# Optimization experiments

Measured on AMD Instinct MI355X. Metric: run time of the kernel, lower is better.

The kernel has to match this reference:

```python
import jax, jax.numpy as jnp
import numpy as np

N_ATOMS = 8000
N_PAIRS = 80000
NF_IN = 32
NF_OUT = 32
N_DIST = 16
N_COMP = 4      # l_max=1: [l=0 (1), l=1 (3)] tensor components
N_INV = 2       # _invariant_counts[(2, 1)]
MIND_SOFT = 0.85
MAXD_SOFT = 5.0
HARD_CUTOFF = 6.5
GN_EPS = 1e-5


def _sensitivity(dist, mu, sigma):
    # HIP-NN style inverse-distance Gaussians with smooth cos^2 cutoff.
    inv_d = 1.0 / dist                                   # (P,)
    base = jnp.exp(-0.5 * ((inv_d[:, None] - mu) / sigma) ** 2)  # (P, n_dist)
    cut = jnp.where(dist < HARD_CUTOFF,
                    jnp.cos(0.5 * jnp.pi * dist / HARD_CUTOFF) ** 2, 0.0)
    return base * cut[:, None]


def setup_inputs() -> dict:
    key = jax.random.key(0)
    ks = jax.random.split(key, 10)
    in_features = jax.random.normal(ks[0], (N_ATOMS, NF_IN), jnp.float32)
    pair_first = jnp.sort(jax.random.randint(ks[1], (N_PAIRS,), 0, N_ATOMS))
    pair_second = jax.random.randint(ks[2], (N_PAIRS,), 0, N_ATOMS)
    dist_pairs = (0.5 + (HARD_CUTOFF - 0.5)
                  * jax.random.uniform(ks[3], (N_PAIRS,), jnp.float32))
    tensor_rhats = jax.random.normal(ks[4], (N_PAIRS, N_COMP), jnp.float32)
    # learned params
    sens_mu = jnp.linspace(1.0 / MAXD_SOFT, 1.0 / MIND_SOFT, N_DIST).astype(jnp.float32)
    sens_sigma = jnp.full((N_DIST,), float(sens_mu[1] - sens_mu[0]), jnp.float32)
    s_int = (2.0 / (N_DIST * NF_IN + NF_OUT)) ** 0.5
    int_weights = s_int * jax.random.normal(ks[5], (N_DIST, NF_OUT, NF_IN), jnp.float32)
    s_self = (2.0 / (NF_IN + NF_OUT)) ** 0.5
    selfint_w = s_self * jax.random.normal(ks[6], (NF_OUT, NF_IN), jnp.float32)
    selfint_b = jnp.zeros((NF_OUT,), jnp.float32)
    s_mix = (2.0 / (N_INV * NF_OUT + NF_OUT)) ** 0.5
    mixing_weights = s_mix * jax.random.normal(ks[7], (NF_OUT, N_INV, NF_OUT), jnp.float32)
    gn_weight = jnp.ones((N_INV * NF_OUT,), jnp.float32)
    gn_bias = jnp.zeros((N_INV * NF_OUT,), jnp.float32)
    return {
        "in_features": in_features, "tensor_rhats": tensor_rhats,
        "dist_pairs": dist_pairs, "int_weights": int_weights,
        "selfint_w": selfint_w, "selfint_b": selfint_b,
        "mixing_weights": mixing_weights, "gn_weight": gn_weight,
        "gn_bias": gn_bias, "sens_mu": sens_mu, "sens_sigma": sens_sigma,
        "pair_first": pair_first, "pair_second": pair_second,
    }


def reference(in_features, tensor_rhats, dist_pairs, int_weights,
              selfint_w, selfint_b, mixing_weights, gn_weight, gn_bias,
              sens_mu, sens_sigma, pair_first, pair_second):
    n_atoms = in_features.shape[0]
    # self interaction (Linear)
    self_part = in_features @ selfint_w.T + selfint_b          # (N, nf_out)
    # tensor sensitivities: (P, n_comp, n_dist) -> flat (P, n_comp*n_dist)
    sense = _sensitivity(dist_pairs, sens_mu, sens_sigma)      # (P, n_dist)
    sense_flat = (tensor_rhats[:, :, None] * sense[:, None, :]).reshape(
        -1, N_COMP * N_DIST)
    # envsum: env[a, s, f] = sum_{p: pair_first[p]=a} sense_flat[p, s] * feat[pair_second[p], f]
    feat_j = in_features[pair_second]                          # (P, nf_in)
    contrib = sense_flat[:, :, None] * feat_j[:, None, :]      # (P, S, nf_in)
    env = jax.ops.segment_sum(contrib, pair_first, num_segments=n_atoms)
    # interaction weights contraction
    w_rs = jnp.transpose(int_weights, (0, 2, 1)).reshape(N_DIST * NF_IN, NF_OUT)
    env_rs = env.reshape(n_atoms * N_COMP, N_DIST * NF_IN)
    tf = (env_rs @ w_rs).reshape(n_atoms, N_COMP, NF_OUT)
    tf = jnp.transpose(tf, (0, 2, 1))                          # (N, nf_out, n_comp)
    # HopInvariantLayer (n_max=2, l_max=1): [l=0 scalar, |l=1 vector|^2]
    invariants = jnp.stack(
        [tf[..., 0], jnp.sum(tf[..., 1:] ** 2, axis=-1)], axis=-1)  # (N, nf_out, 2)
    # GroupNorm over channels (n_inv groups of nf_out channels)
    x = jnp.transpose(invariants, (0, 2, 1))                   # (N, n_inv, nf_out)
    mean = jnp.mean(x, axis=-1, keepdims=True)
    var = jnp.var(x, axis=-1, keepdims=True)
    xn = (x - mean) / jnp.sqrt(var + GN_EPS)
    xn = xn * gn_weight.reshape(N_INV, NF_OUT) + gn_bias.reshape(N_INV, NF_OUT)
    norm_inv = jnp.transpose(xn, (0, 2, 1)).reshape(n_atoms, NF_OUT * N_INV)
    mix = norm_inv @ mixing_weights.reshape(NF_OUT * N_INV, NF_OUT)
    return mix + self_part
```

## Files before the change

kernel.cpp:

```cpp
#include <hip/hip_runtime.h>
#include <hip/hip_bf16.h>
#include <stdint.h>

#define GN_EPS 1e-5f

typedef __fp16 half2_t __attribute__((ext_vector_type(2)));
typedef __fp16 v8h __attribute__((ext_vector_type(8)));
typedef float v4f __attribute__((ext_vector_type(4)));
union U32H2 { uint32_t u; half2_t h; };
union U4V8 { uint4 u; v8h h; };
union UF { uint32_t u; float f; };

__device__ __forceinline__ float ldin(const void* p, int i, bool bf) {
    if (bf) {
        UF c; c.u = ((uint32_t)((const uint16_t*)p)[i]) << 16;
        return c.f;
    }
    return ((const float*)p)[i];
}

__device__ __forceinline__ uint16_t f2bf(float x) {
    union { float f; uint32_t u; } c; c.f = x;
    uint32_t u = c.u;
    return (uint16_t)((u + 0x7FFFu + ((u >> 16) & 1u)) >> 16);
}

__device__ __forceinline__ bool detect_bf16(const void* gnw) {
    uint32_t det = *(const uint32_t*)gnw;
    return (det >> 16) == (det & 0xFFFFu);
}

__device__ __forceinline__ uint32_t pkh2(float lo, float hi) {
    U32H2 u; u.h = __builtin_amdgcn_cvt_pkrtz(lo, hi); return u.u;
}

__global__ __launch_bounds__(256) void k0_prep(
    const void* __restrict__ intw, const void* __restrict__ selfw,
    const void* __restrict__ selfb, const void* __restrict__ mw,
    const void* __restrict__ gnw, const void* __restrict__ gnb,
    const void* __restrict__ mu, const void* __restrict__ sig,
    const int* __restrict__ pf,
    int* __restrict__ seg, uint32_t* __restrict__ Wmf,
    uint32_t* __restrict__ selfh, float* __restrict__ mwT,
    float* __restrict__ gnwf, float* __restrict__ gnbf,
    float* __restrict__ selfbf, float* __restrict__ muf,
    float* __restrict__ isgf, int n_atoms, int n_pairs)
{
    const bool bf = detect_bf16(gnw);
    const int tid = blockIdx.x * 256 + threadIdx.x;

    if (tid < n_pairs) {
        int a0 = pf[tid];
        if (tid == 0) { for (int a = 0; a <= a0; ++a) seg[a] = 0; }
        if (tid + 1 < n_pairs) {
            int a1 = pf[tid + 1];
            for (int a = a0 + 1; a <= a1; ++a) seg[a] = tid + 1;
        } else {
            for (int a = a0 + 1; a <= n_atoms; ++a) seg[a] = n_pairs;
        }
    }
    if (tid < 8192) {
        int fp = tid & 15, d = (tid >> 4) & 15, o = tid >> 8;
        float wlo = ldin(intw, (d * 32 + o) * 32 + 2 * fp, bf);
        float whi = ldin(intw, (d * 32 + o) * 32 + 2 * fp + 1, bf);
        Wmf[tid] = pkh2(wlo, whi);
    }
    if (tid < 512) {
        int fp = tid & 15, o = tid >> 4;
        selfh[tid] = pkh2(ldin(selfw, o * 32 + 2 * fp, bf),
                          ldin(selfw, o * 32 + 2 * fp + 1, bf));
    }
    if (tid < 2048) {
        int k = tid & 63, o = tid >> 6;
        mwT[tid] = ldin(mw, k * 32 + o, bf);
    }
    if (tid < 64) { gnwf[tid] = ldin(gnw, tid, bf); gnbf[tid] = ldin(gnb, tid, bf); }
    if (tid < 32) selfbf[tid] = ldin(selfb, tid, bf);
    if (tid < 16) { muf[tid] = ldin(mu, tid, bf); isgf[tid] = 1.0f / ldin(sig, tid, bf); }
}

template <bool BF>
__device__ __forceinline__ void ldfeat8(const void* feat, int j, int fq, float fj[8]) {
    if (BF) {
        uint4 q = *(const uint4*)((const uint16_t*)feat + (size_t)j * 32 + fq * 8);
        uint32_t qd[4] = {q.x, q.y, q.z, q.w};
#pragma unroll
        for (int k = 0; k < 4; ++k) {
            UF lo, hi; lo.u = qd[k] << 16; hi.u = qd[k] & 0xFFFF0000u;
            fj[2 * k] = lo.f; fj[2 * k + 1] = hi.f;
        }
    } else {
        const float4* fr = (const float4*)((const float*)feat + (size_t)j * 32) + fq * 2;
        float4 a = fr[0], b = fr[1];
        fj[0] = a.x; fj[1] = a.y; fj[2] = a.z; fj[3] = a.w;
        fj[4] = b.x; fj[5] = b.y; fj[6] = b.z; fj[7] = b.w;
    }
}

template <bool BF>
__device__ __forceinline__ void pair_phase(
    const void* __restrict__ feat, const void* __restrict__ rhats,
    const void* __restrict__ dists, const int* __restrict__ ps,
    int s, int e, int fq, float mu_d, float isg_d, float (&env)[4][8])
{
    for (int p = s; p < e; p += 4) {
        int jj[4]; float4 rc[4]; float invd[4];
#pragma unroll
        for (int i = 0; i < 4; ++i) {
            int pi = (p + i < e) ? p + i : e - 1;
            jj[i] = ps[pi];
            float dist, r0, r1, r2, r3;
            if (BF) {
                UF d16; d16.u = ((uint32_t)((const uint16_t*)dists)[pi]) << 16;
                dist = d16.f;
                uint2 rv = *(const uint2*)((const uint16_t*)rhats + 4 * pi);
                UF e0, e1, e2, e3;
                e0.u = rv.x << 16; e1.u = rv.x & 0xFFFF0000u;
                e2.u = rv.y << 16; e3.u = rv.y & 0xFFFF0000u;
                r0 = e0.f; r1 = e1.f; r2 = e2.f; r3 = e3.f;
            } else {
                dist = ((const float*)dists)[pi];
                float4 rv = ((const float4*)rhats)[pi];
                r0 = rv.x; r1 = rv.y; r2 = rv.z; r3 = rv.w;
            }
            float cd = __cosf(0.2416609733530613f * dist);
            float cut = (dist < 6.5f) ? cd * cd : 0.0f;
            if (p + i >= e) cut = 0.0f;
            rc[i] = make_float4(r0 * cut, r1 * cut, r2 * cut, r3 * cut);
            invd[i] = __builtin_amdgcn_rcpf(dist);
        }
        float fj[4][8];
#pragma unroll
        for (int i = 0; i < 4; ++i) ldfeat8<BF>(feat, jj[i], fq, fj[i]);
#pragma unroll
        for (int i = 0; i < 4; ++i) {
            float x = (invd[i] - mu_d) * isg_d;
            float sd = __expf(-0.5f * x * x);
            float t0 = sd * rc[i].x, t1 = sd * rc[i].y;
            float t2 = sd * rc[i].z, t3 = sd * rc[i].w;
#pragma unroll
            for (int fl = 0; fl < 8; ++fl) {
                env[0][fl] = fmaf(t0, fj[i][fl], env[0][fl]);
                env[1][fl] = fmaf(t1, fj[i][fl], env[1][fl]);
                env[2][fl] = fmaf(t2, fj[i][fl], env[2][fl]);
                env[3][fl] = fmaf(t3, fj[i][fl], env[3][fl]);
            }
        }
    }
}

__global__ __launch_bounds__(256, 5) void k2_main(
    const int* __restrict__ seg, const uint32_t* __restrict__ Wmf,
    const uint32_t* __restrict__ selfh, const float* __restrict__ mwT,
    const void* __restrict__ feat, const void* __restrict__ rhats,
    const void* __restrict__ dists, const int* __restrict__ ps,
    const float* __restrict__ gnwf, const float* __restrict__ gnbf,
    const float* __restrict__ selfbf, const float* __restrict__ muf,
    const float* __restrict__ isgf, const void* __restrict__ gnw,
    void* __restrict__ out, int n_atoms)
{
    __shared__ uint32_t envs[16 * 256];
    __shared__ float tfs[4 * 32 * 4];
    __shared__ float selfs[4][32];
    __shared__ float xns[4][64];

    const bool bf = detect_bf16(gnw);
    const int t = threadIdx.x, wv = t >> 6, lane = t & 63;
    const int a0 = blockIdx.x * 4;
    int a = a0 + wv;
    const bool astore = (a < n_atoms);
    if (!astore) a = n_atoms - 1;

    const int dD = lane >> 2, fq = lane & 3;
    const float mu_d = muf[dD], isg_d = isgf[dD];

    float env[4][8];
#pragma unroll
    for (int c = 0; c < 4; ++c)
#pragma unroll
        for (int fl = 0; fl < 8; ++fl) env[c][fl] = 0.0f;

    const int s = seg[a], e = seg[a + 1];
    if (bf) pair_phase<true >(feat, rhats, dists, ps, s, e, fq, mu_d, isg_d, env);
    else    pair_phase<false>(feat, rhats, dists, ps, s, e, fq, mu_d, isg_d, env);

    {
        const int ci = dD * 4 + fq;
#pragma unroll
        for (int c = 0; c < 4; ++c) {
            int m = wv * 4 + c;
            uint4 w;
            w.x = pkh2(env[c][0], env[c][1]);
            w.y = pkh2(env[c][2], env[c][3]);
            w.z = pkh2(env[c][4], env[c][5]);
            w.w = pkh2(env[c][6], env[c][7]);
            *(uint4*)&envs[m * 256 + ((ci ^ m) << 2)] = w;
        }
    }
    __syncthreads();

    const int mrow = lane & 15, quad = lane >> 4;
    const int tile = wv >> 1;
    if ((wv & 1) == 0) {
        v4f acc = {0.f, 0.f, 0.f, 0.f};
        const uint4* wb = (const uint4*)Wmf + ((tile * 16 + mrow) * 64 + quad);
#pragma unroll
        for (int kk = 0; kk < 16; ++kk) {
            int cia = kk * 4 + quad;
            U4V8 Af, Bf;
            Af.u = *(const uint4*)&envs[mrow * 256 + ((cia ^ mrow) << 2)];
            Bf.u = wb[kk * 4];
            acc = __builtin_amdgcn_mfma_f32_16x16x32_f16(Af.h, Bf.h, acc, 0, 0, 0);
        }
        float4 st; st.x = acc[0]; st.y = acc[1]; st.z = acc[2]; st.w = acc[3];
        *(float4*)&tfs[(quad * 32 + tile * 16 + mrow) * 4] = st;
    } else {
        int ar = a0 + (mrow < 4 ? mrow : 0);
        if (ar >= n_atoms) ar = n_atoms - 1;
        U4V8 Af, Bf;
        if (bf) {
            uint4 q = *(const uint4*)((const uint16_t*)feat + (size_t)ar * 32 + quad * 8);
            uint32_t qd[4] = {q.x, q.y, q.z, q.w};
            uint32_t r[4];
#pragma unroll
            for (int k = 0; k < 4; ++k) {
                UF lo, hi; lo.u = qd[k] << 16; hi.u = qd[k] & 0xFFFF0000u;
                r[k] = pkh2(lo.f, hi.f);
            }
            Af.u = make_uint4(r[0], r[1], r[2], r[3]);
        } else {
            const float4* fp4 = (const float4*)((const float*)feat + (size_t)ar * 32 + quad * 8);
            float4 x = fp4[0], y = fp4[1];
            Af.u = make_uint4(pkh2(x.x, x.y), pkh2(x.z, x.w),
                              pkh2(y.x, y.y), pkh2(y.z, y.w));
        }
        Bf.u = *(const uint4*)(selfh + (tile * 16 + mrow) * 16 + quad * 4);
        v4f acc = {0.f, 0.f, 0.f, 0.f};
        acc = __builtin_amdgcn_mfma_f32_16x16x32_f16(Af.h, Bf.h, acc, 0, 0, 0);
        if (quad == 0) {
#pragma unroll
            for (int r = 0; r < 4; ++r)
                selfs[r][tile * 16 + mrow] = acc[r];
        }
    }
    __syncthreads();

    const int o = lane & 31, half = lane >> 5;
    float4 tf = *(const float4*)&tfs[(wv * 32 + o) * 4];
    float inv0 = tf.x;
    float inv1 = tf.y * tf.y + tf.z * tf.z + tf.w * tf.w;

    float s0 = inv0, q0 = inv0 * inv0, s1 = inv1, q1 = inv1 * inv1;
#pragma unroll
    for (int m = 16; m >= 1; m >>= 1) {
        s0 += __shfl_xor(s0, m, 32);
        q0 += __shfl_xor(q0, m, 32);
        s1 += __shfl_xor(s1, m, 32);
        q1 += __shfl_xor(q1, m, 32);
    }
    float mean0 = s0 * (1.f / 32.f), mean1 = s1 * (1.f / 32.f);
    float var0 = q0 * (1.f / 32.f) - mean0 * mean0;
    float var1 = q1 * (1.f / 32.f) - mean1 * mean1;
    float xn0 = (inv0 - mean0) * rsqrtf(var0 + GN_EPS);
    float xn1 = (inv1 - mean1) * rsqrtf(var1 + GN_EPS);
    xn0 = xn0 * gnwf[o] + gnbf[o];
    xn1 = xn1 * gnwf[32 + o] + gnbf[32 + o];

    if (half == 0) *(float2*)&xns[wv][2 * o] = make_float2(xn0, xn1);

    float mix = 0.0f;
    const float4* mrow4 = (const float4*)(mwT + o * 64);
#pragma unroll
    for (int c = 0; c < 16; ++c) {
        float4 xk = *(const float4*)&xns[wv][c * 4];
        float4 w4 = mrow4[c];
        mix = fmaf(xk.x, w4.x, mix);
        mix = fmaf(xk.y, w4.y, mix);
        mix = fmaf(xk.z, w4.z, mix);
        mix = fmaf(xk.w, w4.w, mix);
    }

    float res = mix + selfs[wv][o] + selfbf[o];
    if (half == 0 && astore) {
        if (bf) ((uint16_t*)out)[a * 32 + o] = f2bf(res);
        else    ((float*)out)[a * 32 + o]    = res;
    }
}

extern "C" void kernel_launch(void* const* d_in, const int* in_sizes, int n_in,
                              void* d_out, int out_size, void* d_ws, size_t ws_size,
                              hipStream_t stream) {
    const void* feat  = d_in[0];
    const void* rhats = d_in[1];
    const void* dists = d_in[2];
    const void* intw  = d_in[3];
    const void* selfw = d_in[4];
    const void* selfb = d_in[5];
    const void* mw    = d_in[6];
    const void* gnw   = d_in[7];
    const void* gnb   = d_in[8];
    const void* mu    = d_in[9];
    const void* sig   = d_in[10];
    const int* pf     = (const int*)d_in[11];
    const int* ps     = (const int*)d_in[12];

    const int n_pairs = in_sizes[11];
    const int n_atoms = in_sizes[0] / 32;

    char* ws = (char*)d_ws;
    int*      seg    = (int*)(ws + 0);
    uint32_t* Wmf    = (uint32_t*)(ws + 32768);
    uint32_t* selfh  = (uint32_t*)(ws + 65536);
    float*    mwT    = (float*)(ws + 69632);
    float*    gnwf   = (float*)(ws + 77824);
    float*    gnbf   = (float*)(ws + 78080);
    float*    selfbf = (float*)(ws + 78336);
    float*    muf    = (float*)(ws + 78464);
    float*    isgf   = (float*)(ws + 78528);

    int thr = n_pairs < 8192 ? 8192 : n_pairs;
    hipLaunchKernelGGL(k0_prep, dim3((thr + 255) / 256), dim3(256), 0, stream,
                       intw, selfw, selfb, mw, gnw, gnb, mu, sig, pf,
                       seg, Wmf, selfh, mwT, gnwf, gnbf, selfbf, muf, isgf,
                       n_atoms, n_pairs);
    hipLaunchKernelGGL(k2_main, dim3((n_atoms + 3) / 4), dim3(256), 0, stream,
                       seg, Wmf, selfh, mwT, feat, rhats, dists, ps,
                       gnwf, gnbf, selfbf, muf, isgf, gnw, d_out, n_atoms);
}
```

Before: 116.8 us.

## Fuse prep kernel into main kernel with binary-search segment bounds

Removes the separate prep kernel. Each wave now finds its atom's pair range by binary search over the sorted pair_first array, and weights are read and converted to fp16 directly from the raw inputs inside the main kernel. This drops one launch and the serial dependency between the two kernels. In exchange it adds redundant per-block weight conversion, global loads in the MFMA loop, a less efficient scalar mixing loop, and lowers the occupancy hint from 5 to 4.

```diff
diff --git a/kernel.cpp b/kernel.cpp
--- a/kernel.cpp
+++ b/kernel.cpp
@@ -34,49 +34,24 @@
     U32H2 u; u.h = __builtin_amdgcn_cvt_pkrtz(lo, hi); return u.u;
 }
 
-__global__ __launch_bounds__(256) void k0_prep(
-    const void* __restrict__ intw, const void* __restrict__ selfw,
-    const void* __restrict__ selfb, const void* __restrict__ mw,
-    const void* __restrict__ gnw, const void* __restrict__ gnb,
-    const void* __restrict__ mu, const void* __restrict__ sig,
-    const int* __restrict__ pf,
-    int* __restrict__ seg, uint32_t* __restrict__ Wmf,
-    uint32_t* __restrict__ selfh, float* __restrict__ mwT,
-    float* __restrict__ gnwf, float* __restrict__ gnbf,
-    float* __restrict__ selfbf, float* __restrict__ muf,
-    float* __restrict__ isgf, int n_atoms, int n_pairs)
-{
-    const bool bf = detect_bf16(gnw);
-    const int tid = blockIdx.x * 256 + threadIdx.x;
-
-    if (tid < n_pairs) {
-        int a0 = pf[tid];
-        if (tid == 0) { for (int a = 0; a <= a0; ++a) seg[a] = 0; }
-        if (tid + 1 < n_pairs) {
-            int a1 = pf[tid + 1];
-            for (int a = a0 + 1; a <= a1; ++a) seg[a] = tid + 1;
-        } else {
-            for (int a = a0 + 1; a <= n_atoms; ++a) seg[a] = n_pairs;
-        }
-    }
-    if (tid < 8192) {
-        int fp = tid & 15, d = (tid >> 4) & 15, o = tid >> 8;
-        float wlo = ldin(intw, (d * 32 + o) * 32 + 2 * fp, bf);
-        float whi = ldin(intw, (d * 32 + o) * 32 + 2 * fp + 1, bf);
-        Wmf[tid] = pkh2(wlo, whi);
-    }
-    if (tid < 512) {
-        int fp = tid & 15, o = tid >> 4;
-        selfh[tid] = pkh2(ldin(selfw, o * 32 + 2 * fp, bf),
-                          ldin(selfw, o * 32 + 2 * fp + 1, bf));
-    }
-    if (tid < 2048) {
-        int k = tid & 63, o = tid >> 6;
-        mwT[tid] = ldin(mw, k * 32 + o, bf);
-    }
-    if (tid < 64) { gnwf[tid] = ldin(gnw, tid, bf); gnbf[tid] = ldin(gnb, tid, bf); }
-    if (tid < 32) selfbf[tid] = ldin(selfb, tid, bf);
-    if (tid < 16) { muf[tid] = ldin(mu, tid, bf); isgf[tid] = 1.0f / ldin(sig, tid, bf); }
+template <bool BF>
+__device__ __forceinline__ uint4 ldrow16(const void* w, int row, int quad) {
+    if (BF) {
+        uint4 q = *(const uint4*)((const uint16_t*)w + (size_t)row * 32 + quad * 8);
+        uint32_t qd[4] = {q.x, q.y, q.z, q.w};
+        uint32_t r[4];
+#pragma unroll
+        for (int k = 0; k < 4; ++k) {
+            UF lo, hi; lo.u = qd[k] << 16; hi.u = qd[k] & 0xFFFF0000u;
+            r[k] = pkh2(lo.f, hi.f);
+        }
+        return make_uint4(r[0], r[1], r[2], r[3]);
+    } else {
+        const float4* f = (const float4*)((const float*)w + (size_t)row * 32 + quad * 8);
+        float4 x = f[0], y = f[1];
+        return make_uint4(pkh2(x.x, x.y), pkh2(x.z, x.w),
+                          pkh2(y.x, y.y), pkh2(y.z, y.w));
+    }
 }
 
 template <bool BF>
@@ -149,15 +124,15 @@
     }
 }
 
-__global__ __launch_bounds__(256, 5) void k2_main(
-    const int* __restrict__ seg, const uint32_t* __restrict__ Wmf,
-    const uint32_t* __restrict__ selfh, const float* __restrict__ mwT,
+__global__ __launch_bounds__(256, 4) void k_all(
     const void* __restrict__ feat, const void* __restrict__ rhats,
-    const void* __restrict__ dists, const int* __restrict__ ps,
-    const float* __restrict__ gnwf, const float* __restrict__ gnbf,
-    const float* __restrict__ selfbf, const float* __restrict__ muf,
-    const float* __restrict__ isgf, const void* __restrict__ gnw,
-    void* __restrict__ out, int n_atoms)
+    const void* __restrict__ dists, const void* __restrict__ intw,
+    const void* __restrict__ selfw, const void* __restrict__ selfb,
+    const void* __restrict__ mw, const void* __restrict__ gnw,
+    const void* __restrict__ gnb, const void* __restrict__ mu,
+    const void* __restrict__ sig, const int* __restrict__ pf,
+    const int* __restrict__ ps, void* __restrict__ out,
+    int n_atoms, int n_pairs)
 {
     __shared__ uint32_t envs[16 * 256];
     __shared__ float tfs[4 * 32 * 4];
@@ -171,8 +146,21 @@
     const bool astore = (a < n_atoms);
     if (!astore) a = n_atoms - 1;
 
+    int s, e;
+    {
+        int target = a + (lane & 1);
+        int lo = 0, hi = n_pairs;
+        while (lo < hi) {
+            int mid = (lo + hi) >> 1;
+            if (pf[mid] < target) lo = mid + 1; else hi = mid;
+        }
+        s = __shfl(lo, 0, 64);
+        e = __shfl(lo, 1, 64);
+    }
+
     const int dD = lane >> 2, fq = lane & 3;
-    const float mu_d = muf[dD], isg_d = isgf[dD];
+    const float mu_d = ldin(mu, dD, bf);
+    const float isg_d = 1.0f / ldin(sig, dD, bf);
 
     float env[4][8];
 #pragma unroll
@@ -180,7 +168,6 @@
 #pragma unroll
         for (int fl = 0; fl < 8; ++fl) env[c][fl] = 0.0f;
 
-    const int s = seg[a], e = seg[a + 1];
     if (bf) pair_phase<true >(feat, rhats, dists, ps, s, e, fq, mu_d, isg_d, env);
     else    pair_phase<false>(feat, rhats, dists, ps, s, e, fq, mu_d, isg_d, env);
 
@@ -201,46 +188,32 @@
 
     const int mrow = lane & 15, quad = lane >> 4;
     const int tile = wv >> 1;
+    const int og = tile * 16 + mrow;
     if ((wv & 1) == 0) {
         v4f acc = {0.f, 0.f, 0.f, 0.f};
-        const uint4* wb = (const uint4*)Wmf + ((tile * 16 + mrow) * 64 + quad);
 #pragma unroll
         for (int kk = 0; kk < 16; ++kk) {
             int cia = kk * 4 + quad;
             U4V8 Af, Bf;
             Af.u = *(const uint4*)&envs[mrow * 256 + ((cia ^ mrow) << 2)];
-            Bf.u = wb[kk * 4];
+            Bf.u = bf ? ldrow16<true >(intw, kk * 32 + og, quad)
+                      : ldrow16<false>(intw, kk * 32 + og, quad);
             acc = __builtin_amdgcn_mfma_f32_16x16x32_f16(Af.h, Bf.h, acc, 0, 0, 0);
         }
         float4 st; st.x = acc[0]; st.y = acc[1]; st.z = acc[2]; st.w = acc[3];
-        *(float4*)&tfs[(quad * 32 + tile * 16 + mrow) * 4] = st;
+        *(float4*)&tfs[(quad * 32 + og) * 4] = st;
     } else {
         int ar = a0 + (mrow < 4 ? mrow : 0);
         if (ar >= n_atoms) ar = n_atoms - 1;
         U4V8 Af, Bf;
-        if (bf) {
-            uint4 q = *(const uint4*)((const uint16_t*)feat + (size_t)ar * 32 + quad * 8);
-            uint32_t qd[4] = {q.x, q.y, q.z, q.w};
-            uint32_t r[4];
-#pragma unroll
-            for (int k = 0; k < 4; ++k) {
-                UF lo, hi; lo.u = qd[k] << 16; hi.u = qd[k] & 0xFFFF0000u;
-                r[k] = pkh2(lo.f, hi.f);
-            }
-            Af.u = make_uint4(r[0], r[1], r[2], r[3]);
-        } else {
-            const float4* fp4 = (const float4*)((const float*)feat + (size_t)ar * 32 + quad * 8);
-            float4 x = fp4[0], y = fp4[1];
-            Af.u = make_uint4(pkh2(x.x, x.y), pkh2(x.z, x.w),
-                              pkh2(y.x, y.y), pkh2(y.z, y.w));
-        }
-        Bf.u = *(const uint4*)(selfh + (tile * 16 + mrow) * 16 + quad * 4);
+        Af.u = bf ? ldrow16<true >(feat, ar, quad) : ldrow16<false>(feat, ar, quad);
+        Bf.u = bf ? ldrow16<true >(selfw, og, quad) : ldrow16<false>(selfw, og, quad);
         v4f acc = {0.f, 0.f, 0.f, 0.f};
         acc = __builtin_amdgcn_mfma_f32_16x16x32_f16(Af.h, Bf.h, acc, 0, 0, 0);
         if (quad == 0) {
 #pragma unroll
             for (int r = 0; r < 4; ++r)
-                selfs[r][tile * 16 + mrow] = acc[r];
+                selfs[r][og] = acc[r];
         }
     }
     __syncthreads();
@@ -263,24 +236,18 @@
     float var1 = q1 * (1.f / 32.f) - mean1 * mean1;
     float xn0 = (inv0 - mean0) * rsqrtf(var0 + GN_EPS);
     float xn1 = (inv1 - mean1) * rsqrtf(var1 + GN_EPS);
-    xn0 = xn0 * gnwf[o] + gnbf[o];
-    xn1 = xn1 * gnwf[32 + o] + gnbf[32 + o];
+    xn0 = xn0 * ldin(gnw, o, bf) + ldin(gnb, o, bf);
+    xn1 = xn1 * ldin(gnw, 32 + o, bf) + ldin(gnb, 32 + o, bf);
 
     if (half == 0) *(float2*)&xns[wv][2 * o] = make_float2(xn0, xn1);
 
     float mix = 0.0f;
-    const float4* mrow4 = (const float4*)(mwT + o * 64);
-#pragma unroll
-    for (int c = 0; c < 16; ++c) {
-        float4 xk = *(const float4*)&xns[wv][c * 4];
-        float4 w4 = mrow4[c];
-        mix = fmaf(xk.x, w4.x, mix);
-        mix = fmaf(xk.y, w4.y, mix);
-        mix = fmaf(xk.z, w4.z, mix);
-        mix = fmaf(xk.w, w4.w, mix);
-    }
-
-    float res = mix + selfs[wv][o] + selfbf[o];
+#pragma unroll 4
+    for (int k = 0; k < 64; ++k) {
+        mix = fmaf(xns[wv][k], ldin(mw, k * 32 + o, bf), mix);
+    }
+
+    float res = mix + selfs[wv][o] + ldin(selfb, o, bf);
     if (half == 0 && astore) {
         if (bf) ((uint16_t*)out)[a * 32 + o] = f2bf(res);
         else    ((float*)out)[a * 32 + o]    = res;
@@ -307,23 +274,7 @@
     const int n_pairs = in_sizes[11];
     const int n_atoms = in_sizes[0] / 32;
 
-    char* ws = (char*)d_ws;
-    int*      seg    = (int*)(ws + 0);
-    uint32_t* Wmf    = (uint32_t*)(ws + 32768);
-    uint32_t* selfh  = (uint32_t*)(ws + 65536);
-    float*    mwT    = (float*)(ws + 69632);
-    float*    gnwf   = (float*)(ws + 77824);
-    float*    gnbf   = (float*)(ws + 78080);
-    float*    selfbf = (float*)(ws + 78336);
-    float*    muf    = (float*)(ws + 78464);
-    float*    isgf   = (float*)(ws + 78528);
-
-    int thr = n_pairs < 8192 ? 8192 : n_pairs;
-    hipLaunchKernelGGL(k0_prep, dim3((thr + 255) / 256), dim3(256), 0, stream,
-                       intw, selfw, selfb, mw, gnw, gnb, mu, sig, pf,
-                       seg, Wmf, selfh, mwT, gnwf, gnbf, selfbf, muf, isgf,
-                       n_atoms, n_pairs);
-    hipLaunchKernelGGL(k2_main, dim3((n_atoms + 3) / 4), dim3(256), 0, stream,
-                       seg, Wmf, selfh, mwT, feat, rhats, dists, ps,
-                       gnwf, gnbf, selfbf, muf, isgf, gnw, d_out, n_atoms);
-}
+    hipLaunchKernelGGL(k_all, dim3((n_atoms + 3) / 4), dim3(256), 0, stream,
+                       feat, rhats, dists, intw, selfw, selfb, mw, gnw, gnb,
+                       mu, sig, pf, ps, d_out, n_atoms, n_pairs);
+}
```

Result: slower. 122.4 us (+4.8%).
